# Performance work log

Hardware: AMD Instinct MI355X
Metric: run time of the kernel (lower is better)

## Reference

```python
import jax, jax.numpy as jnp
import numpy as np

E, D, H, B = 8, 64, 512, 32768  # n_experts, state_dim, hidden width, batch
IN = D + 3  # x, t, sin(omega*t), cos(omega*t)


def setup_inputs() -> dict:
    key = jax.random.key(0)
    ks = jax.random.split(key, 12)
    s = 0.02
    return {
        "t": jax.random.uniform(ks[0], (1,), dtype=jnp.float32),
        "x": jax.random.normal(ks[1], (B, D), dtype=jnp.float32),
        "expert_weights": jax.random.uniform(ks[2], (B, E), dtype=jnp.float32),
        "omega": jnp.arange(1, E + 1, dtype=jnp.float32),  # omega_i = i+1
        "W1": jax.random.normal(ks[3], (E, H, IN), dtype=jnp.float32) * s,
        "b1": jnp.zeros((E, H), dtype=jnp.float32),
        "W2": jax.random.normal(ks[4], (E, H, H), dtype=jnp.float32) * s,
        "b2": jnp.zeros((E, H), dtype=jnp.float32),
        "W3": jax.random.normal(ks[5], (E, H, H), dtype=jnp.float32) * s,
        "b3": jnp.zeros((E, H), dtype=jnp.float32),
        "W4": jax.random.normal(ks[6], (E, D, H), dtype=jnp.float32) * s,
        "b4": jnp.zeros((E, D), dtype=jnp.float32),
    }


def reference(t, x, expert_weights, omega, W1, b1, W2, b2, W3, b3, W4, b4):
    # Dense path of ExpertODEEnsemble.forward: all experts active.
    nB = x.shape[0]
    tb = jnp.broadcast_to(t, (nB,))                       # (B,)
    wt = omega[:, None] * tb[None, :]                     # (E, B)
    # Per-expert inputs: [x, t, sin(wt), cos(wt)] -> (E, B, D+3)
    xe = jnp.broadcast_to(x[None], (E, nB, D))
    te = jnp.broadcast_to(tb[None, :, None], (E, nB, 1))
    inp = jnp.concatenate([xe, te, jnp.sin(wt)[..., None], jnp.cos(wt)[..., None]], axis=-1)
    h = jnp.tanh(jnp.einsum('ebi,ehi->ebh', inp, W1) + b1[:, None, :])
    h = jnp.tanh(jnp.einsum('ebh,egh->ebg', h, W2) + b2[:, None, :])
    h = jnp.tanh(jnp.einsum('ebh,egh->ebg', h, W3) + b3[:, None, :])
    dyn = jnp.einsum('ebh,edh->ebd', h, W4) + b4[:, None, :]   # (E, B, D)
    # Weighted combine: sum_e w[b,e] * dyn[e,b,:]
    dx_dt = jnp.einsum('be,ebd->bd', expert_weights, dyn)
    return dx_dt
```

## Files before the change

### kernel.cpp

```cpp
#include <hip/hip_runtime.h>
#include <hip/hip_bf16.h>


typedef unsigned short ushort_t;
typedef unsigned int u32;
typedef unsigned long long u64;
typedef __attribute__((ext_vector_type(8))) short short8;
typedef __attribute__((ext_vector_type(4))) float floatx4;
typedef __attribute__((ext_vector_type(16))) float floatx16;
typedef __attribute__((ext_vector_type(4))) int intx4;

#define W1A_OFF 0u
#define W2A_OFF 524288u
#define W3A_OFF 4718592u
#define W4A_OFF 8912896u
#define XB_OFF  9437184u
#define B1E_OFF 13631488u

#define X_OFF_L 135168
#define SYNC_OFF 152064
#define SMEM_SZ 152128

static __device__ __forceinline__ u32 pk2bf(float a, float b) {
  union { __hip_bfloat162 h; u32 u; } v;
  v.h = __float22bfloat162_rn(make_float2(a, b));
  return v.u;
}

static __device__ __forceinline__ float pade_tanh(float x) {
  float x2 = x * x;
  float num = __builtin_fmaf(x2, __builtin_fmaf(x2, 1.0f, 105.0f), 945.0f);
  float den = __builtin_fmaf(x2, __builtin_fmaf(x2, 15.0f, 420.0f), 945.0f);
  return x * num * __builtin_amdgcn_rcpf(den);
}

static __device__ __forceinline__ void ald16(const void* g, void* l) {
  __builtin_amdgcn_global_load_lds((__attribute__((address_space(1))) void*)g,
                                   (__attribute__((address_space(3))) void*)l,
                                   16, 0, 0);
}

static __device__ __forceinline__ floatx16 mfma32(short8 a, short8 b, floatx16 c) {
  return __builtin_amdgcn_mfma_f32_32x32x16_bf16(a, b, c, 0, 0, 0);
}

static __device__ __forceinline__ void waitge(const int* p, int tgt) {
  while (*(volatile const int*)p < tgt) __builtin_amdgcn_s_sleep(1);
  __asm__ __volatile__("" ::: "memory");
}

static __device__ __forceinline__ void bump(int* p, int lane) {
  __asm__ __volatile__("s_waitcnt lgkmcnt(0)" ::: "memory");
  if (lane == 0) atomicAdd(p, 1);
}

__global__ __launch_bounds__(256) void prep_kernel(
    const float* __restrict__ t, const float* __restrict__ x,
    const float* __restrict__ omega, const float* __restrict__ W1,
    const float* __restrict__ b1, const float* __restrict__ W2,
    const float* __restrict__ W3, const float* __restrict__ W4,
    char* __restrict__ ws) {
  int i = blockIdx.x * 256 + threadIdx.x;
  if (i < 32768) {
    int e = i >> 12, d = i & 4095;
    int lane = d & 63, q = d >> 6;
    int ol = q & 1, kc = (q >> 1) & 3, w = q >> 3;
    int outr = w * 64 + ol * 32 + (lane & 31);
    int kg = kc * 2 + (lane >> 5);
    const float* s = W1 + (e * 512 + outr) * 67 + kg * 8;
    ((intx4*)(ws + W1A_OFF))[i] = (intx4){
        (int)pk2bf(s[0], s[1]), (int)pk2bf(s[2], s[3]),
        (int)pk2bf(s[4], s[5]), (int)pk2bf(s[6], s[7])};
    return;
  }
  i -= 32768;
  if (i < 262144) {
    int e = i >> 15, d = i & 32767;
    int lane = d & 63, q = d >> 6;
    int ol = q & 1, kc = (q >> 1) & 31, w = q >> 6;
    int outr = w * 64 + ol * 32 + (lane & 31);
    int kg = kc * 2 + (lane >> 5);
    const floatx4* s = (const floatx4*)(W2 + ((e << 9) + outr) * 512 + (kg << 3));
    floatx4 lo = s[0], hi = s[1];
    ((intx4*)(ws + W2A_OFF))[i] = (intx4){
        (int)pk2bf(lo[0], lo[1]), (int)pk2bf(lo[2], lo[3]),
        (int)pk2bf(hi[0], hi[1]), (int)pk2bf(hi[2], hi[3])};
    return;
  }
  i -= 262144;
  if (i < 262144) {
    int e = i >> 15, d = i & 32767;
    int lane = d & 63, q = d >> 6;
    int ol = q & 1, kc = (q >> 1) & 31, w = q >> 6;
    int outr = w * 64 + ol * 32 + (lane & 31);
    int kg = kc * 2 + (lane >> 5);
    const floatx4* s = (const floatx4*)(W3 + ((e << 9) + outr) * 512 + (kg << 3));
    floatx4 lo = s[0], hi = s[1];
    ((intx4*)(ws + W3A_OFF))[i] = (intx4){
        (int)pk2bf(lo[0], lo[1]), (int)pk2bf(lo[2], lo[3]),
        (int)pk2bf(hi[0], hi[1]), (int)pk2bf(hi[2], hi[3])};
    return;
  }
  i -= 262144;
  if (i < 32768) {
    int e = i >> 12, d = i & 4095;
    int lane = d & 63, q = d >> 6;
    int kc = q & 31, o4 = q >> 5;
    int outr = o4 * 32 + (lane & 31);
    int kg = kc * 2 + (lane >> 5);
    const floatx4* s = (const floatx4*)(W4 + ((e << 6) + outr) * 512 + (kg << 3));
    floatx4 lo = s[0], hi = s[1];
    ((intx4*)(ws + W4A_OFF))[i] = (intx4){
        (int)pk2bf(lo[0], lo[1]), (int)pk2bf(lo[2], lo[3]),
        (int)pk2bf(hi[0], hi[1]), (int)pk2bf(hi[2], hi[3])};
    return;
  }
  i -= 32768;
  if (i < 262144) {
    const floatx4* s = (const floatx4*)(x + i * 8);
    floatx4 lo = s[0], hi = s[1];
    ((intx4*)(ws + XB_OFF))[i] = (intx4){
        (int)pk2bf(lo[0], lo[1]), (int)pk2bf(lo[2], lo[3]),
        (int)pk2bf(hi[0], hi[1]), (int)pk2bf(hi[2], hi[3])};
    return;
  }
  i -= 262144;
  if (i < 4096) {
    float tv = t[0];
    int e = i >> 9;
    float om = omega[e];
    ((float*)(ws + B1E_OFF))[i] = b1[i] + tv * W1[i * 67 + 64]
        + sinf(om * tv) * W1[i * 67 + 65] + cosf(om * tv) * W1[i * 67 + 66];
  }
}


template <int NKC, bool ISX>
static __device__ __forceinline__ void mlp_layer(
    const char* __restrict__ bsrc, char* __restrict__ act,
    int* kcp, int* pub, int lane, int w, int q1, int r31,
    const char* __restrict__ Abase, const float* __restrict__ bias,
    int pub_tgt, int tgt_cov, int tgt_oth, int khm, bool do_epi_wait) {
  const int voff = lane * 16;
  const char* sp = Abase + w * (NKC * 2048) + voff;

  floatx16 acc[2][4];
#pragma unroll
  for (int ol = 0; ol < 2; ++ol) {
    int fe0 = w * 64 + ol * 32 + 4 * q1;
#pragma unroll
    for (int g = 0; g < 4; ++g) {
      floatx4 bv = *(const floatx4*)(bias + fe0 + 8 * g);
#pragma unroll
      for (int nt = 0; nt < 4; ++nt) {
        acc[ol][nt][4 * g + 0] = bv[0];
        acc[ol][nt][4 * g + 1] = bv[1];
        acc[ol][nt][4 * g + 2] = bv[2];
        acc[ol][nt][4 * g + 3] = bv[3];
      }
    }
  }
  short8 a0 = *(const short8*)(sp);
  short8 a1 = *(const short8*)(sp + 1024);
  sp += 2048;

  const int NG = NKC / 4;
#pragma unroll 1
  for (int g = 0; g < NG; ++g) {
    if (!ISX) waitge(pub + g, pub_tgt);
    const char* gb = bsrc + g * (4 * 4224) + voff;
    short8 b0 = *(const short8*)(gb);
    short8 b1v = *(const short8*)(gb + 1024);
    short8 b2 = *(const short8*)(gb + 2048);
    short8 b3 = *(const short8*)(gb + 3072);
#pragma unroll
    for (int j = 0; j < 4; ++j) {
      short8 an0 = *(const short8*)(sp);
      short8 an1 = *(const short8*)(sp + 1024);
      sp += 2048;
      const char* bn = gb + ((j + 1) & 3) * 4224;
      short8 bn0 = *(const short8*)(bn);
      short8 bn1 = *(const short8*)(bn + 1024);
      short8 bn2 = *(const short8*)(bn + 2048);
      short8 bn3 = *(const short8*)(bn + 3072);
      acc[0][0] = mfma32(a0, b0, acc[0][0]);
      acc[0][1] = mfma32(a0, b1v, acc[0][1]);
      acc[0][2] = mfma32(a0, b2, acc[0][2]);
      acc[0][3] = mfma32(a0, b3, acc[0][3]);
      acc[1][0] = mfma32(a1, b0, acc[1][0]);
      acc[1][1] = mfma32(a1, b1v, acc[1][1]);
      acc[1][2] = mfma32(a1, b2, acc[1][2]);
      acc[1][3] = mfma32(a1, b3, acc[1][3]);
      a0 = an0; a1 = an1;
      b0 = bn0; b1v = bn1; b2 = bn2; b3 = bn3;
    }
    bump(kcp + w, lane);
  }

  if (do_epi_wait) {
    for (int w2 = 0; w2 < 8; ++w2)
      waitge(kcp + w2, ((w2 >> 2) == khm) ? tgt_cov : tgt_oth);
  }
#pragma unroll
  for (int ol = 0; ol < 2; ++ol) {
#pragma unroll
    for (int g = 0; g < 4; ++g) {
      int ko = ol * 4 + g;
      char* base = act + (4 * w + (ko >> 1)) * 4224
                   + (((ko & 1) * 32 + r31) << 4) + q1 * 8;
#pragma unroll
      for (int nt = 0; nt < 4; ++nt) {
        float v0 = pade_tanh(acc[ol][nt][4 * g + 0]);
        float v1 = pade_tanh(acc[ol][nt][4 * g + 1]);
        float v2 = pade_tanh(acc[ol][nt][4 * g + 2]);
        float v3 = pade_tanh(acc[ol][nt][4 * g + 3]);
        u32 lo = pk2bf(v0, v1), hi = pk2bf(v2, v3);
        *(u64*)(base + nt * 1024) = ((u64)hi << 32) | lo;
      }
    }
  }
  bump(pub + w, lane);
}

extern "C" __global__ __launch_bounds__(512) void fused_kernel(
    const char* __restrict__ ws, const float* __restrict__ b2,
    const float* __restrict__ b3, const float* __restrict__ b4,
    const float* __restrict__ ew, float* __restrict__ out) {
  extern __shared__ char smem[];
  char* act = smem;
  char* xreg = smem + X_OFF_L;
  int* kcp = (int*)(smem + SYNC_OFF);
  int* pub = kcp + 8;

  const int t = threadIdx.x, lane = t & 63, w = t >> 6;
  const int q1 = lane >> 5, r31 = lane & 31;
  const int row0 = blockIdx.x << 7;
  const int voff = lane * 16;

  if (t < 16) ((int*)(smem + SYNC_OFF))[t] = 0;

  const ushort_t* xb = (const ushort_t*)(ws + XB_OFF);
#pragma unroll
  for (int s = 0; s < 2; ++s) {
    int u = w + 8 * s, v = u >> 2, nt = u & 3;
    ald16(xb + (row0 + nt * 32 + r31) * 64 + (2 * v + q1) * 8,
          xreg + v * 4224 + nt * 1024);
  }
  __syncthreads();

  const int rt = w & 3, kh = w >> 2;
  const int row_l4 = row0 + rt * 32 + r31;
  floatx16 oacc[2] = {};

  for (int e = 0; e < 8; ++e) {
    mlp_layer<4, true>(xreg, act, kcp, pub, lane, w, q1, r31,
                       ws + W1A_OFF + e * 65536,
                       (const float*)(ws + B1E_OFF) + e * 512,
                       0, 21 * e + (w & 3) - 3, 21 * e + w - 11, w >> 2, e > 0);
    mlp_layer<32, false>(act, act, kcp, pub, lane, w, q1, r31,
                         ws + W2A_OFF + e * 524288, b2 + e * 512,
                         3 * e + 1, 21 * e + w + 2, 21 * e + w + 2, 0, true);
    mlp_layer<32, false>(act, act, kcp, pub, lane, w, q1, r31,
                         ws + W3A_OFF + e * 524288, b3 + e * 512,
                         3 * e + 2, 21 * e + w + 10, 21 * e + w + 10, 0, true);

    {
      const char* spA = ws + W4A_OFF + e * 65536 + voff;
      const float sc = ew[row_l4 * 8 + e];
      floatx16 acc4[2] = {};
      int kc0 = kh * 16;
      short8 a0 = *(const short8*)(spA + kc0 * 1024);
      short8 a1 = *(const short8*)(spA + 32768 + kc0 * 1024);
#pragma unroll 1
      for (int gl = 0; gl < 4; ++gl) {
        int g = kh * 4 + gl;
        waitge(pub + g, 3 * e + 3);
        const char* gb = act + g * (4 * 4224) + rt * 1024 + voff;
        short8 b = *(const short8*)(gb);
#pragma unroll
        for (int j = 0; j < 4; ++j) {
          int kc = g * 4 + j;
          short8 an0 = *(const short8*)(spA + (kc + 1) * 1024);
          short8 an1 = *(const short8*)(spA + 32768 + (kc + 1) * 1024);
          short8 bn = *(const short8*)(gb + ((j + 1) & 3) * 4224);
          acc4[0] = mfma32(a0, b, acc4[0]);
          acc4[1] = mfma32(a1, b, acc4[1]);
          a0 = an0; a1 = an1; b = bn;
        }
        bump(kcp + w, lane);
      }
      if (kh == 0) {
        const float* bp = b4 + e * 64;
#pragma unroll
        for (int ol = 0; ol < 2; ++ol) {
          int fe0 = ol * 32 + 4 * q1;
#pragma unroll
          for (int g = 0; g < 4; ++g) {
            floatx4 bv = *(const floatx4*)(bp + fe0 + 8 * g);
            oacc[ol][4 * g + 0] += sc * (acc4[ol][4 * g + 0] + bv[0]);
            oacc[ol][4 * g + 1] += sc * (acc4[ol][4 * g + 1] + bv[1]);
            oacc[ol][4 * g + 2] += sc * (acc4[ol][4 * g + 2] + bv[2]);
            oacc[ol][4 * g + 3] += sc * (acc4[ol][4 * g + 3] + bv[3]);
          }
        }
      } else {
#pragma unroll
        for (int ol = 0; ol < 2; ++ol)
#pragma unroll
          for (int i = 0; i < 16; ++i) oacc[ol][i] += sc * acc4[ol][i];
      }
    }
  }

  __syncthreads();
  if (kh == 1) {
#pragma unroll
    for (int ol = 0; ol < 2; ++ol)
#pragma unroll
      for (int g = 0; g < 4; ++g) {
        floatx4 p = {oacc[ol][4 * g + 0], oacc[ol][4 * g + 1],
                     oacc[ol][4 * g + 2], oacc[ol][4 * g + 3]};
        *(floatx4*)(act + rt * 8192 + ol * 4096 + g * 1024 + lane * 16) = p;
      }
  }
  __syncthreads();
  if (kh == 0) {
    float* orow = out + row_l4 * 64;
#pragma unroll
    for (int ol = 0; ol < 2; ++ol)
#pragma unroll
      for (int g = 0; g < 4; ++g) {
        floatx4 p = *(const floatx4*)(act + rt * 8192 + ol * 4096 + g * 1024 + lane * 16);
        floatx4 v = {oacc[ol][4 * g + 0] + p[0], oacc[ol][4 * g + 1] + p[1],
                     oacc[ol][4 * g + 2] + p[2], oacc[ol][4 * g + 3] + p[3]};
        *(floatx4*)(orow + ol * 32 + 8 * g + 4 * q1) = v;
      }
  }
}

extern "C" void kernel_launch(void* const* d_in, const int* in_sizes, int n_in,
                              void* d_out, int out_size, void* d_ws, size_t ws_size,
                              hipStream_t stream) {
  const float* t  = (const float*)d_in[0];
  const float* x  = (const float*)d_in[1];
  const float* ew = (const float*)d_in[2];
  const float* om = (const float*)d_in[3];
  const float* W1 = (const float*)d_in[4];
  const float* b1 = (const float*)d_in[5];
  const float* W2 = (const float*)d_in[6];
  const float* b2 = (const float*)d_in[7];
  const float* W3 = (const float*)d_in[8];
  const float* b3 = (const float*)d_in[9];
  const float* W4 = (const float*)d_in[10];
  const float* b4 = (const float*)d_in[11];
  char* ws = (char*)d_ws;
  float* out = (float*)d_out;
  (void)in_sizes; (void)n_in; (void)ws_size; (void)out_size;

  static int smem_set = 0;
  if (!smem_set) {
    hipFuncSetAttribute((const void*)fused_kernel,
                        hipFuncAttributeMaxDynamicSharedMemorySize, SMEM_SZ);
    smem_set = 1;
  }
  prep_kernel<<<3344, 256, 0, stream>>>(t, x, om, W1, b1, W2, W3, W4, ws);
  fused_kernel<<<256, 512, SMEM_SZ, stream>>>(ws, b2, b3, b4, ew, out);
}
```

Measured before the change: 431.3 us.

## Split fused MLP into 64-row, 4-wave blocks with two blocks per CU

The fused expert-MLP kernel now uses blocks of 256 threads covering 64 rows instead of 512 threads covering 128 rows. Each wave computes 128 output features against two 32-row tiles, and LDS use is roughly halved so two blocks fit per CU. The inter-wave counters and epilogue waits are reworked to match: the W4 stage reads only slabs the wave wrote itself, and the final cross-wave reduction sums four partials. The aim is better latency hiding through more resident blocks and less cross-wave waiting. The cost is twice as many blocks, each streaming the full bf16 weight set from L2, so weight reuse per block drops.

```diff
diff --git a/kernel.cpp b/kernel.cpp
--- a/kernel.cpp
+++ b/kernel.cpp
@@ -17,9 +17,10 @@
 #define XB_OFF  9437184u
 #define B1E_OFF 13631488u
 
-#define X_OFF_L 135168
-#define SYNC_OFF 152064
-#define SMEM_SZ 152128
+#define SLAB 2112
+#define X_OFF_L 67584
+#define SYNC_OFF 76032
+#define SMEM_SZ 76096
 
 static __device__ __forceinline__ u32 pk2bf(float a, float b) {
   union { __hip_bfloat162 h; u32 u; } v;
@@ -134,25 +135,25 @@
   }
 }
 
-
-template <int NKC, bool ISX>
-static __device__ __forceinline__ void mlp_layer(
+template <int NKC, bool ISX, bool BUMP>
+static __device__ __forceinline__ void mlp_layer4(
     const char* __restrict__ bsrc, char* __restrict__ act,
     int* kcp, int* pub, int lane, int w, int q1, int r31,
     const char* __restrict__ Abase, const float* __restrict__ bias,
-    int pub_tgt, int tgt_cov, int tgt_oth, int khm, bool do_epi_wait) {
+    int pub_tgt, int epi_base, bool do_epi) {
   const int voff = lane * 16;
-  const char* sp = Abase + w * (NKC * 2048) + voff;
-
-  floatx16 acc[2][4];
-#pragma unroll
-  for (int ol = 0; ol < 2; ++ol) {
-    int fe0 = w * 64 + ol * 32 + 4 * q1;
+  const int AH = NKC * 2048;
+  const char* spA = Abase + (2 * w) * AH + voff;
+
+  floatx16 acc[4][2];
+#pragma unroll
+  for (int ol = 0; ol < 4; ++ol) {
+    int fe0 = w * 128 + ol * 32 + 4 * q1;
 #pragma unroll
     for (int g = 0; g < 4; ++g) {
       floatx4 bv = *(const floatx4*)(bias + fe0 + 8 * g);
 #pragma unroll
-      for (int nt = 0; nt < 4; ++nt) {
+      for (int nt = 0; nt < 2; ++nt) {
         acc[ol][nt][4 * g + 0] = bv[0];
         acc[ol][nt][4 * g + 1] = bv[1];
         acc[ol][nt][4 * g + 2] = bv[2];
@@ -160,56 +161,56 @@
       }
     }
   }
-  short8 a0 = *(const short8*)(sp);
-  short8 a1 = *(const short8*)(sp + 1024);
-  sp += 2048;
+  short8 a0 = *(const short8*)(spA);
+  short8 a1 = *(const short8*)(spA + 1024);
+  short8 a2 = *(const short8*)(spA + AH);
+  short8 a3 = *(const short8*)(spA + AH + 1024);
+  spA += 2048;
 
   const int NG = NKC / 4;
 #pragma unroll 1
   for (int g = 0; g < NG; ++g) {
-    if (!ISX) waitge(pub + g, pub_tgt);
-    const char* gb = bsrc + g * (4 * 4224) + voff;
+    if (!ISX) waitge(pub + (g >> 1), pub_tgt);
+    const char* gb = bsrc + g * (4 * SLAB) + voff;
     short8 b0 = *(const short8*)(gb);
     short8 b1v = *(const short8*)(gb + 1024);
-    short8 b2 = *(const short8*)(gb + 2048);
-    short8 b3 = *(const short8*)(gb + 3072);
 #pragma unroll
     for (int j = 0; j < 4; ++j) {
-      short8 an0 = *(const short8*)(sp);
-      short8 an1 = *(const short8*)(sp + 1024);
-      sp += 2048;
-      const char* bn = gb + ((j + 1) & 3) * 4224;
+      short8 an0 = *(const short8*)(spA);
+      short8 an1 = *(const short8*)(spA + 1024);
+      short8 an2 = *(const short8*)(spA + AH);
+      short8 an3 = *(const short8*)(spA + AH + 1024);
+      spA += 2048;
+      const char* bn = gb + ((j + 1) & 3) * SLAB;
       short8 bn0 = *(const short8*)(bn);
       short8 bn1 = *(const short8*)(bn + 1024);
-      short8 bn2 = *(const short8*)(bn + 2048);
-      short8 bn3 = *(const short8*)(bn + 3072);
       acc[0][0] = mfma32(a0, b0, acc[0][0]);
       acc[0][1] = mfma32(a0, b1v, acc[0][1]);
-      acc[0][2] = mfma32(a0, b2, acc[0][2]);
-      acc[0][3] = mfma32(a0, b3, acc[0][3]);
       acc[1][0] = mfma32(a1, b0, acc[1][0]);
       acc[1][1] = mfma32(a1, b1v, acc[1][1]);
-      acc[1][2] = mfma32(a1, b2, acc[1][2]);
-      acc[1][3] = mfma32(a1, b3, acc[1][3]);
-      a0 = an0; a1 = an1;
-      b0 = bn0; b1v = bn1; b2 = bn2; b3 = bn3;
-    }
-    bump(kcp + w, lane);
-  }
-
-  if (do_epi_wait) {
-    for (int w2 = 0; w2 < 8; ++w2)
-      waitge(kcp + w2, ((w2 >> 2) == khm) ? tgt_cov : tgt_oth);
-  }
-#pragma unroll
-  for (int ol = 0; ol < 2; ++ol) {
+      acc[2][0] = mfma32(a2, b0, acc[2][0]);
+      acc[2][1] = mfma32(a2, b1v, acc[2][1]);
+      acc[3][0] = mfma32(a3, b0, acc[3][0]);
+      acc[3][1] = mfma32(a3, b1v, acc[3][1]);
+      a0 = an0; a1 = an1; a2 = an2; a3 = an3;
+      b0 = bn0; b1v = bn1;
+    }
+    if (BUMP) bump(kcp + w, lane);
+  }
+
+  if (do_epi) {
+#pragma unroll 1
+    for (int w2 = 0; w2 < 4; ++w2) waitge(kcp + w2, epi_base + 2 * w + 2);
+  }
+#pragma unroll
+  for (int ol = 0; ol < 4; ++ol) {
 #pragma unroll
     for (int g = 0; g < 4; ++g) {
       int ko = ol * 4 + g;
-      char* base = act + (4 * w + (ko >> 1)) * 4224
+      char* base = act + (8 * w + (ko >> 1)) * SLAB
                    + (((ko & 1) * 32 + r31) << 4) + q1 * 8;
 #pragma unroll
-      for (int nt = 0; nt < 4; ++nt) {
+      for (int nt = 0; nt < 2; ++nt) {
         float v0 = pade_tanh(acc[ol][nt][4 * g + 0]);
         float v1 = pade_tanh(acc[ol][nt][4 * g + 1]);
         float v2 = pade_tanh(acc[ol][nt][4 * g + 2]);
@@ -222,7 +223,7 @@
   bump(pub + w, lane);
 }
 
-extern "C" __global__ __launch_bounds__(512) void fused_kernel(
+extern "C" __global__ __launch_bounds__(256, 2) void fused_kernel(
     const char* __restrict__ ws, const float* __restrict__ b2,
     const float* __restrict__ b3, const float* __restrict__ b4,
     const float* __restrict__ ew, float* __restrict__ out) {
@@ -230,111 +231,119 @@
   char* act = smem;
   char* xreg = smem + X_OFF_L;
   int* kcp = (int*)(smem + SYNC_OFF);
-  int* pub = kcp + 8;
+  int* pub = kcp + 4;
 
   const int t = threadIdx.x, lane = t & 63, w = t >> 6;
   const int q1 = lane >> 5, r31 = lane & 31;
-  const int row0 = blockIdx.x << 7;
+  const int row0 = blockIdx.x << 6;
   const int voff = lane * 16;
 
-  if (t < 16) ((int*)(smem + SYNC_OFF))[t] = 0;
+  if (t < 8) ((int*)(smem + SYNC_OFF))[t] = 0;
 
   const ushort_t* xb = (const ushort_t*)(ws + XB_OFF);
 #pragma unroll
   for (int s = 0; s < 2; ++s) {
-    int u = w + 8 * s, v = u >> 2, nt = u & 3;
+    int u = w + 4 * s, v = u >> 1, nt = u & 1;
     ald16(xb + (row0 + nt * 32 + r31) * 64 + (2 * v + q1) * 8,
-          xreg + v * 4224 + nt * 1024);
+          xreg + v * SLAB + nt * 1024);
   }
   __syncthreads();
 
-  const int rt = w & 3, kh = w >> 2;
-  const int row_l4 = row0 + rt * 32 + r31;
-  floatx16 oacc[2] = {};
+  floatx16 oacc[2][2] = {};
 
   for (int e = 0; e < 8; ++e) {
-    mlp_layer<4, true>(xreg, act, kcp, pub, lane, w, q1, r31,
-                       ws + W1A_OFF + e * 65536,
-                       (const float*)(ws + B1E_OFF) + e * 512,
-                       0, 21 * e + (w & 3) - 3, 21 * e + w - 11, w >> 2, e > 0);
-    mlp_layer<32, false>(act, act, kcp, pub, lane, w, q1, r31,
-                         ws + W2A_OFF + e * 524288, b2 + e * 512,
-                         3 * e + 1, 21 * e + w + 2, 21 * e + w + 2, 0, true);
-    mlp_layer<32, false>(act, act, kcp, pub, lane, w, q1, r31,
-                         ws + W3A_OFF + e * 524288, b3 + e * 512,
-                         3 * e + 2, 21 * e + w + 10, 21 * e + w + 10, 0, true);
+    mlp_layer4<4, true, false>(xreg, act, kcp, pub, lane, w, q1, r31,
+                               ws + W1A_OFF + e * 65536,
+                               (const float*)(ws + B1E_OFF) + e * 512,
+                               0, 0, false);
+    mlp_layer4<32, false, true>(act, act, kcp, pub, lane, w, q1, r31,
+                                ws + W2A_OFF + e * 524288, b2 + e * 512,
+                                3 * e + 1, 16 * e, true);
+    mlp_layer4<32, false, true>(act, act, kcp, pub, lane, w, q1, r31,
+                                ws + W3A_OFF + e * 524288, b3 + e * 512,
+                                3 * e + 2, 16 * e + 8, true);
 
     {
       const char* spA = ws + W4A_OFF + e * 65536 + voff;
-      const float sc = ew[row_l4 * 8 + e];
-      floatx16 acc4[2] = {};
-      int kc0 = kh * 16;
+      floatx16 acc4[2][2] = {};
+      const int kc0 = 8 * w;
       short8 a0 = *(const short8*)(spA + kc0 * 1024);
-      short8 a1 = *(const short8*)(spA + 32768 + kc0 * 1024);
+      short8 a1 = *(const short8*)(spA + (32 + kc0) * 1024);
 #pragma unroll 1
-      for (int gl = 0; gl < 4; ++gl) {
-        int g = kh * 4 + gl;
-        waitge(pub + g, 3 * e + 3);
-        const char* gb = act + g * (4 * 4224) + rt * 1024 + voff;
-        short8 b = *(const short8*)(gb);
+      for (int gl = 0; gl < 2; ++gl) {
+        int g = 2 * w + gl;
+        const char* gb = act + g * (4 * SLAB) + voff;
+        short8 b0 = *(const short8*)(gb);
+        short8 b1v = *(const short8*)(gb + 1024);
 #pragma unroll
         for (int j = 0; j < 4; ++j) {
-          int kc = g * 4 + j;
+          int kc = kc0 + gl * 4 + j;
           short8 an0 = *(const short8*)(spA + (kc + 1) * 1024);
-          short8 an1 = *(const short8*)(spA + 32768 + (kc + 1) * 1024);
-          short8 bn = *(const short8*)(gb + ((j + 1) & 3) * 4224);
-          acc4[0] = mfma32(a0, b, acc4[0]);
-          acc4[1] = mfma32(a1, b, acc4[1]);
-          a0 = an0; a1 = an1; b = bn;
+          short8 an1 = *(const short8*)(spA + (33 + kc) * 1024);
+          const char* bn = gb + ((j + 1) & 3) * SLAB;
+          short8 bn0 = *(const short8*)(bn);
+          short8 bn1 = *(const short8*)(bn + 1024);
+          acc4[0][0] = mfma32(a0, b0, acc4[0][0]);
+          acc4[0][1] = mfma32(a0, b1v, acc4[0][1]);
+          acc4[1][0] = mfma32(a1, b0, acc4[1][0]);
+          acc4[1][1] = mfma32(a1, b1v, acc4[1][1]);
+          a0 = an0; a1 = an1; b0 = bn0; b1v = bn1;
         }
-        bump(kcp + w, lane);
-      }
-      if (kh == 0) {
-        const float* bp = b4 + e * 64;
-#pragma unroll
-        for (int ol = 0; ol < 2; ++ol) {
-          int fe0 = ol * 32 + 4 * q1;
-#pragma unroll
-          for (int g = 0; g < 4; ++g) {
-            floatx4 bv = *(const floatx4*)(bp + fe0 + 8 * g);
-            oacc[ol][4 * g + 0] += sc * (acc4[ol][4 * g + 0] + bv[0]);
-            oacc[ol][4 * g + 1] += sc * (acc4[ol][4 * g + 1] + bv[1]);
-            oacc[ol][4 * g + 2] += sc * (acc4[ol][4 * g + 2] + bv[2]);
-            oacc[ol][4 * g + 3] += sc * (acc4[ol][4 * g + 3] + bv[3]);
+      }
+#pragma unroll
+      for (int nt = 0; nt < 2; ++nt) {
+        const float sc = ew[(row0 + nt * 32 + r31) * 8 + e];
+        if (w == 0) {
+          const float* bp = b4 + e * 64;
+#pragma unroll
+          for (int o4 = 0; o4 < 2; ++o4) {
+            int fe0 = o4 * 32 + 4 * q1;
+#pragma unroll
+            for (int g = 0; g < 4; ++g) {
+              floatx4 bv = *(const floatx4*)(bp + fe0 + 8 * g);
+              oacc[o4][nt][4 * g + 0] += sc * (acc4[o4][nt][4 * g + 0] + bv[0]);
+              oacc[o4][nt][4 * g + 1] += sc * (acc4[o4][nt][4 * g + 1] + bv[1]);
+              oacc[o4][nt][4 * g + 2] += sc * (acc4[o4][nt][4 * g + 2] + bv[2]);
+              oacc[o4][nt][4 * g + 3] += sc * (acc4[o4][nt][4 * g + 3] + bv[3]);
+            }
           }
+        } else {
+#pragma unroll
+          for (int o4 = 0; o4 < 2; ++o4)
+#pragma unroll
+            for (int i = 0; i < 16; ++i)
+              oacc[o4][nt][i] += sc * acc4[o4][nt][i];
         }
-      } else {
-#pragma unroll
-        for (int ol = 0; ol < 2; ++ol)
-#pragma unroll
-          for (int i = 0; i < 16; ++i) oacc[ol][i] += sc * acc4[ol][i];
       }
     }
   }
 
   __syncthreads();
-  if (kh == 1) {
-#pragma unroll
-    for (int ol = 0; ol < 2; ++ol)
+#pragma unroll
+  for (int o4 = 0; o4 < 2; ++o4)
+#pragma unroll
+    for (int nt = 0; nt < 2; ++nt)
 #pragma unroll
       for (int g = 0; g < 4; ++g) {
-        floatx4 p = {oacc[ol][4 * g + 0], oacc[ol][4 * g + 1],
-                     oacc[ol][4 * g + 2], oacc[ol][4 * g + 3]};
-        *(floatx4*)(act + rt * 8192 + ol * 4096 + g * 1024 + lane * 16) = p;
-      }
-  }
+        floatx4 p = {oacc[o4][nt][4 * g + 0], oacc[o4][nt][4 * g + 1],
+                     oacc[o4][nt][4 * g + 2], oacc[o4][nt][4 * g + 3]};
+        *(floatx4*)(act + (w * 4096 + (nt * 32 + r31) * 64
+                           + o4 * 32 + g * 8 + q1 * 4) * 4) = p;
+      }
   __syncthreads();
-  if (kh == 0) {
-    float* orow = out + row_l4 * 64;
-#pragma unroll
-    for (int ol = 0; ol < 2; ++ol)
-#pragma unroll
-      for (int g = 0; g < 4; ++g) {
-        floatx4 p = *(const floatx4*)(act + rt * 8192 + ol * 4096 + g * 1024 + lane * 16);
-        floatx4 v = {oacc[ol][4 * g + 0] + p[0], oacc[ol][4 * g + 1] + p[1],
-                     oacc[ol][4 * g + 2] + p[2], oacc[ol][4 * g + 3] + p[3]};
-        *(floatx4*)(orow + ol * 32 + 8 * g + 4 * q1) = v;
-      }
+  {
+    float* orow = out + row0 * 64;
+#pragma unroll
+    for (int k = 0; k < 4; ++k) {
+      int f = w * 1024 + k * 256 + lane * 4;
+      floatx4 s0 = *(const floatx4*)(act + f * 4);
+      floatx4 s1 = *(const floatx4*)(act + (4096 + f) * 4);
+      floatx4 s2 = *(const floatx4*)(act + (8192 + f) * 4);
+      floatx4 s3 = *(const floatx4*)(act + (12288 + f) * 4);
+      floatx4 v = {s0[0] + s1[0] + s2[0] + s3[0], s0[1] + s1[1] + s2[1] + s3[1],
+                   s0[2] + s1[2] + s2[2] + s3[2], s0[3] + s1[3] + s2[3] + s3[3]};
+      *(floatx4*)(orow + f) = v;
+    }
   }
 }
 
@@ -364,5 +373,5 @@
     smem_set = 1;
   }
   prep_kernel<<<3344, 256, 0, stream>>>(t, x, om, W1, b1, W2, W3, W4, ws);
-  fused_kernel<<<256, 512, SMEM_SZ, stream>>>(ws, b2, b3, b4, ew, out);
-}
+  fused_kernel<<<512, 256, SMEM_SZ, stream>>>(ws, b2, b3, b4, ew, out);
+}
```

New measurement: 686.7 us. +59.2%, slower.

## Rotate activation buffers across nine LDS slots with staggered per-wave K order

Applied to the files above, without the earlier changes.

Replaces the in-place activation buffer with a nine-slot rotating LDS ring, so each layer writes into a fresh slot and no longer waits for every wave to finish reading the previous one. Each wave starts its K loop at its own published group and walks backward, using finer per-group counters and vectorised guard checks in place of full barrier-like waits. Layer 1 now reads x directly from global memory instead of staging it in LDS. MFMA issue is raised with setprio and waves are staggered at start with sleeps. The synchronisation protocol is intricate and raises the risk of races or deadlock.

```diff
diff --git a/kernel.cpp b/kernel.cpp
--- a/kernel.cpp
+++ b/kernel.cpp
@@ -17,9 +17,9 @@
 #define XB_OFF  9437184u
 #define B1E_OFF 13631488u
 
-#define X_OFF_L 135168
-#define SYNC_OFF 152064
-#define SMEM_SZ 152128
+#define SLOTB 16384
+#define SYNC_OFF 147456
+#define SMEM_SZ 147552
 
 static __device__ __forceinline__ u32 pk2bf(float a, float b) {
   union { __hip_bfloat162 h; u32 u; } v;
@@ -34,14 +34,14 @@
   return x * num * __builtin_amdgcn_rcpf(den);
 }
 
-static __device__ __forceinline__ void ald16(const void* g, void* l) {
-  __builtin_amdgcn_global_load_lds((__attribute__((address_space(1))) void*)g,
-                                   (__attribute__((address_space(3))) void*)l,
-                                   16, 0, 0);
-}
-
 static __device__ __forceinline__ floatx16 mfma32(short8 a, short8 b, floatx16 c) {
   return __builtin_amdgcn_mfma_f32_32x32x16_bf16(a, b, c, 0, 0, 0);
+}
+
+static __device__ __forceinline__ int slot9(int g, int b) {
+  int s = g + b;
+  if (s >= 9) s -= 9;
+  return s * SLOTB;
 }
 
 static __device__ __forceinline__ void waitge(const int* p, int tgt) {
@@ -49,8 +49,43 @@
   __asm__ __volatile__("" ::: "memory");
 }
 
+static __device__ __forceinline__ void waitge4(const int* p, int tgt) {
+  for (;;) {
+    __asm__ __volatile__("" ::: "memory");
+    intx4 v = *(const intx4*)p;
+    if (v[0] >= tgt && v[1] >= tgt && v[2] >= tgt && v[3] >= tgt) break;
+    __builtin_amdgcn_s_sleep(1);
+  }
+  __asm__ __volatile__("" ::: "memory");
+}
+
+static __device__ __forceinline__ void guard_grp(const int* grp, int w, int base) {
+  int tg0 = base + ((0 - w - 1) & 7) + 1;
+  int tg1 = base + ((1 - w - 1) & 7) + 1;
+  int tg2 = base + ((2 - w - 1) & 7) + 1;
+  int tg3 = base + ((3 - w - 1) & 7) + 1;
+  int tg4 = base + ((4 - w - 1) & 7) + 1;
+  int tg5 = base + ((5 - w - 1) & 7) + 1;
+  int tg6 = base + ((6 - w - 1) & 7) + 1;
+  int tg7 = base + ((7 - w - 1) & 7) + 1;
+  for (;;) {
+    __asm__ __volatile__("" ::: "memory");
+    intx4 a = *(const intx4*)grp;
+    intx4 b = *(const intx4*)(grp + 4);
+    if (a[0] >= tg0 && a[1] >= tg1 && a[2] >= tg2 && a[3] >= tg3 &&
+        b[0] >= tg4 && b[1] >= tg5 && b[2] >= tg6 && b[3] >= tg7) break;
+    __builtin_amdgcn_s_sleep(1);
+  }
+  __asm__ __volatile__("" ::: "memory");
+}
+
 static __device__ __forceinline__ void bump(int* p, int lane) {
   __asm__ __volatile__("s_waitcnt lgkmcnt(0)" ::: "memory");
+  if (lane == 0) atomicAdd(p, 1);
+}
+
+static __device__ __forceinline__ void bump_sig(int* p, int lane) {
+  __builtin_amdgcn_sched_barrier(0);
   if (lane == 0) atomicAdd(p, 1);
 }
 
@@ -135,14 +170,35 @@
 }
 
 
-template <int NKC, bool ISX>
-static __device__ __forceinline__ void mlp_layer(
-    const char* __restrict__ bsrc, char* __restrict__ act,
-    int* kcp, int* pub, int lane, int w, int q1, int r31,
+static __device__ __forceinline__ void epi_write(
+    floatx16 acc[2][4], char* __restrict__ act, int wbyte, int r31, int q1) {
+#pragma unroll
+  for (int ol = 0; ol < 2; ++ol) {
+#pragma unroll
+    for (int g = 0; g < 4; ++g) {
+      int ko = ol * 4 + g;
+      char* base = act + wbyte + (ko >> 1) * 4096
+                   + (((ko & 1) * 32 + r31) << 4) + q1 * 8;
+#pragma unroll
+      for (int nt = 0; nt < 4; ++nt) {
+        float v0 = pade_tanh(acc[ol][nt][4 * g + 0]);
+        float v1 = pade_tanh(acc[ol][nt][4 * g + 1]);
+        float v2 = pade_tanh(acc[ol][nt][4 * g + 2]);
+        float v3 = pade_tanh(acc[ol][nt][4 * g + 3]);
+        u32 lo = pk2bf(v0, v1), hi = pk2bf(v2, v3);
+        *(u64*)(base + nt * 1024) = ((u64)hi << 32) | lo;
+      }
+    }
+  }
+}
+
+static __device__ __forceinline__ void mlp_l1(
+    char* __restrict__ act, int* pub, int* l4c, int* grp,
+    int lane, int w, int q1, int r31,
     const char* __restrict__ Abase, const float* __restrict__ bias,
-    int pub_tgt, int tgt_cov, int tgt_oth, int khm, bool do_epi_wait) {
+    const char* __restrict__ xl, int wbyte, int e) {
   const int voff = lane * 16;
-  const char* sp = Abase + w * (NKC * 2048) + voff;
+  const char* ap = Abase + w * 8192 + voff;
 
   floatx16 acc[2][4];
 #pragma unroll
@@ -160,29 +216,105 @@
       }
     }
   }
-  short8 a0 = *(const short8*)(sp);
-  short8 a1 = *(const short8*)(sp + 1024);
-  sp += 2048;
-
-  const int NG = NKC / 4;
+  short8 b0 = *(const short8*)(xl);
+  short8 b1v = *(const short8*)(xl + 4096);
+  short8 b2 = *(const short8*)(xl + 8192);
+  short8 b3 = *(const short8*)(xl + 12288);
+  short8 a0 = *(const short8*)(ap);
+  short8 a1 = *(const short8*)(ap + 1024);
+
+#pragma unroll
+  for (int j = 0; j < 4; ++j) {
+    int kcn = (j < 3) ? (j + 1) : 3;
+    const char* xn = xl + kcn * 32;
+    const char* apn = (j < 3) ? (ap + 2048) : ap;
+    short8 an0 = *(const short8*)(apn);
+    short8 an1 = *(const short8*)(apn + 1024);
+    short8 bn0 = *(const short8*)(xn);
+    short8 bn1 = *(const short8*)(xn + 4096);
+    short8 bn2 = *(const short8*)(xn + 8192);
+    short8 bn3 = *(const short8*)(xn + 12288);
+    __builtin_amdgcn_s_setprio(1);
+    acc[0][0] = mfma32(a0, b0, acc[0][0]);
+    acc[0][1] = mfma32(a0, b1v, acc[0][1]);
+    acc[0][2] = mfma32(a0, b2, acc[0][2]);
+    acc[0][3] = mfma32(a0, b3, acc[0][3]);
+    acc[1][0] = mfma32(a1, b0, acc[1][0]);
+    acc[1][1] = mfma32(a1, b1v, acc[1][1]);
+    acc[1][2] = mfma32(a1, b2, acc[1][2]);
+    acc[1][3] = mfma32(a1, b3, acc[1][3]);
+    __builtin_amdgcn_s_setprio(0);
+    a0 = an0; a1 = an1;
+    b0 = bn0; b1v = bn1; b2 = bn2; b3 = bn3;
+    ap = apn;
+  }
+  if (e > 0) {
+    if (w < 7) waitge4(l4c + ((w + 1) >> 2) * 4, e);
+    else       guard_grp(grp, w, 16 * e - 8);
+  }
+  epi_write(acc, act, wbyte, r31, q1);
+  bump(pub + w, lane);
+}
+
+static __device__ __forceinline__ void mlp_mid(
+    char* __restrict__ act, int* pub, int* grp, int lane, int w, int q1, int r31,
+    const char* __restrict__ Abase, const float* __restrict__ bias,
+    int pub_tgt, int rbase9, int wbyte, int gmode, int garg,
+    const int* __restrict__ l4p) {
+  const int voff = lane * 16;
+  const char* spA = Abase + w * 65536 + voff;
+
+  floatx16 acc[2][4];
+#pragma unroll
+  for (int ol = 0; ol < 2; ++ol) {
+    int fe0 = w * 64 + ol * 32 + 4 * q1;
+#pragma unroll
+    for (int g = 0; g < 4; ++g) {
+      floatx4 bv = *(const floatx4*)(bias + fe0 + 8 * g);
+#pragma unroll
+      for (int nt = 0; nt < 4; ++nt) {
+        acc[ol][nt][4 * g + 0] = bv[0];
+        acc[ol][nt][4 * g + 1] = bv[1];
+        acc[ol][nt][4 * g + 2] = bv[2];
+        acc[ol][nt][4 * g + 3] = bv[3];
+      }
+    }
+  }
+  const char* gb = act + slot9(w, rbase9) + voff;
+  const char* ap = spA + (4 * w) * 2048;
+  short8 b0 = *(const short8*)(gb);
+  short8 b1v = *(const short8*)(gb + 1024);
+  short8 b2 = *(const short8*)(gb + 2048);
+  short8 b3 = *(const short8*)(gb + 3072);
+  short8 a0 = *(const short8*)(ap);
+  short8 a1 = *(const short8*)(ap + 1024);
+
 #pragma unroll 1
-  for (int g = 0; g < NG; ++g) {
-    if (!ISX) waitge(pub + g, pub_tgt);
-    const char* gb = bsrc + g * (4 * 4224) + voff;
-    short8 b0 = *(const short8*)(gb);
-    short8 b1v = *(const short8*)(gb + 1024);
-    short8 b2 = *(const short8*)(gb + 2048);
-    short8 b3 = *(const short8*)(gb + 3072);
+  for (int i = 0; i < 8; ++i) {
 #pragma unroll
     for (int j = 0; j < 4; ++j) {
-      short8 an0 = *(const short8*)(sp);
-      short8 an1 = *(const short8*)(sp + 1024);
-      sp += 2048;
-      const char* bn = gb + ((j + 1) & 3) * 4224;
-      short8 bn0 = *(const short8*)(bn);
-      short8 bn1 = *(const short8*)(bn + 1024);
-      short8 bn2 = *(const short8*)(bn + 2048);
-      short8 bn3 = *(const short8*)(bn + 3072);
+      const char* apn;
+      const char* gbn = gb;
+      const char* bsl;
+      if (j < 3) {
+        apn = ap + 2048;
+        bsl = gb + (j + 1) * 4096;
+      } else if (i < 7) {
+        int g2 = (w - i - 1) & 7;
+        waitge(pub + g2, pub_tgt);
+        gbn = act + slot9(g2, rbase9) + voff;
+        apn = spA + (4 * g2) * 2048;
+        bsl = gbn;
+      } else {
+        apn = ap; bsl = gb;
+      }
+      short8 an0 = *(const short8*)(apn);
+      short8 an1 = *(const short8*)(apn + 1024);
+      short8 bn0 = *(const short8*)(bsl);
+      short8 bn1 = *(const short8*)(bsl + 1024);
+      short8 bn2 = *(const short8*)(bsl + 2048);
+      short8 bn3 = *(const short8*)(bsl + 3072);
+      __builtin_amdgcn_s_setprio(1);
       acc[0][0] = mfma32(a0, b0, acc[0][0]);
       acc[0][1] = mfma32(a0, b1v, acc[0][1]);
       acc[0][2] = mfma32(a0, b2, acc[0][2]);
@@ -191,34 +323,17 @@
       acc[1][1] = mfma32(a1, b1v, acc[1][1]);
       acc[1][2] = mfma32(a1, b2, acc[1][2]);
       acc[1][3] = mfma32(a1, b3, acc[1][3]);
+      __builtin_amdgcn_s_setprio(0);
       a0 = an0; a1 = an1;
       b0 = bn0; b1v = bn1; b2 = bn2; b3 = bn3;
+      ap = apn; gb = gbn;
     }
-    bump(kcp + w, lane);
-  }
-
-  if (do_epi_wait) {
-    for (int w2 = 0; w2 < 8; ++w2)
-      waitge(kcp + w2, ((w2 >> 2) == khm) ? tgt_cov : tgt_oth);
-  }
-#pragma unroll
-  for (int ol = 0; ol < 2; ++ol) {
-#pragma unroll
-    for (int g = 0; g < 4; ++g) {
-      int ko = ol * 4 + g;
-      char* base = act + (4 * w + (ko >> 1)) * 4224
-                   + (((ko & 1) * 32 + r31) << 4) + q1 * 8;
-#pragma unroll
-      for (int nt = 0; nt < 4; ++nt) {
-        float v0 = pade_tanh(acc[ol][nt][4 * g + 0]);
-        float v1 = pade_tanh(acc[ol][nt][4 * g + 1]);
-        float v2 = pade_tanh(acc[ol][nt][4 * g + 2]);
-        float v3 = pade_tanh(acc[ol][nt][4 * g + 3]);
-        u32 lo = pk2bf(v0, v1), hi = pk2bf(v2, v3);
-        *(u64*)(base + nt * 1024) = ((u64)hi << 32) | lo;
-      }
-    }
-  }
+    bump_sig(grp + w, lane);
+  }
+
+  if (gmode == 1)      guard_grp(grp, w, garg);
+  else if (gmode == 2) waitge4(l4p, garg);
+  epi_write(acc, act, wbyte, r31, q1);
   bump(pub + w, lane);
 }
 
@@ -228,79 +343,99 @@
     const float* __restrict__ ew, float* __restrict__ out) {
   extern __shared__ char smem[];
   char* act = smem;
-  char* xreg = smem + X_OFF_L;
-  int* kcp = (int*)(smem + SYNC_OFF);
-  int* pub = kcp + 8;
+  int* l4c = (int*)(smem + SYNC_OFF);
+  int* pub = l4c + 8;
+  int* grp = l4c + 16;
 
   const int t = threadIdx.x, lane = t & 63, w = t >> 6;
   const int q1 = lane >> 5, r31 = lane & 31;
   const int row0 = blockIdx.x << 7;
   const int voff = lane * 16;
 
-  if (t < 16) ((int*)(smem + SYNC_OFF))[t] = 0;
-
-  const ushort_t* xb = (const ushort_t*)(ws + XB_OFF);
-#pragma unroll
-  for (int s = 0; s < 2; ++s) {
-    int u = w + 8 * s, v = u >> 2, nt = u & 3;
-    ald16(xb + (row0 + nt * 32 + r31) * 64 + (2 * v + q1) * 8,
-          xreg + v * 4224 + nt * 1024);
-  }
+  if (t < 24) ((int*)(smem + SYNC_OFF))[t] = 0;
   __syncthreads();
+
+  for (int i = (7 - w) * 7; i > 0; --i) __builtin_amdgcn_s_sleep(1);
+
+  const char* xl = (const char*)ws + XB_OFF + (size_t)row0 * 128
+                   + r31 * 128 + q1 * 16;
 
   const int rt = w & 3, kh = w >> 2;
   const int row_l4 = row0 + rt * 32 + r31;
   floatx16 oacc[2] = {};
 
   for (int e = 0; e < 8; ++e) {
-    mlp_layer<4, true>(xreg, act, kcp, pub, lane, w, q1, r31,
-                       ws + W1A_OFF + e * 65536,
-                       (const float*)(ws + B1E_OFF) + e * 512,
-                       0, 21 * e + (w & 3) - 3, 21 * e + w - 11, w >> 2, e > 0);
-    mlp_layer<32, false>(act, act, kcp, pub, lane, w, q1, r31,
-                         ws + W2A_OFF + e * 524288, b2 + e * 512,
-                         3 * e + 1, 21 * e + w + 2, 21 * e + w + 2, 0, true);
-    mlp_layer<32, false>(act, act, kcp, pub, lane, w, q1, r31,
-                         ws + W3A_OFF + e * 524288, b3 + e * 512,
-                         3 * e + 2, 21 * e + w + 10, 21 * e + w + 10, 0, true);
+    int l0 = 3 * e;
+    int s1 = (l0 + 1) % 9, s2 = (l0 + 2) % 9, s3 = (l0 + 3) % 9;
+
+    mlp_l1(act, pub, l4c, grp, lane, w, q1, r31,
+           (const char*)ws + W1A_OFF + e * 65536,
+           (const float*)(ws + B1E_OFF) + e * 512, xl, slot9(w, s1), e);
+    mlp_mid(act, pub, grp, lane, w, q1, r31,
+            (const char*)ws + W2A_OFF + e * 524288, b2 + e * 512,
+            3 * e + 1, s1, slot9(w, s2),
+            (w < 7) ? 1 : ((e > 0) ? 2 : 0),
+            (w < 7) ? 16 * e : e, l4c);
+    mlp_mid(act, pub, grp, lane, w, q1, r31,
+            (const char*)ws + W3A_OFF + e * 524288, b3 + e * 512,
+            3 * e + 2, s2, slot9(w, s3),
+            1, (w < 7) ? 16 * e + 8 : 16 * e, l4c);
 
     {
-      const char* spA = ws + W4A_OFF + e * 65536 + voff;
+      const char* spA4 = (const char*)ws + W4A_OFF + e * 65536 + voff;
       const float sc = ew[row_l4 * 8 + e];
       floatx16 acc4[2] = {};
-      int kc0 = kh * 16;
-      short8 a0 = *(const short8*)(spA + kc0 * 1024);
-      short8 a1 = *(const short8*)(spA + 32768 + kc0 * 1024);
+      int g = 4 * kh + 3;
+      waitge(pub + g, 3 * e + 3);
+      const char* agb = spA4 + (4 * g) * 1024;
+      const char* gb = act + slot9(g, s3) + rt * 1024 + voff;
+      short8 a0 = *(const short8*)(agb);
+      short8 a1 = *(const short8*)(agb + 32768);
+      short8 b = *(const short8*)(gb);
 #pragma unroll 1
       for (int gl = 0; gl < 4; ++gl) {
-        int g = kh * 4 + gl;
-        waitge(pub + g, 3 * e + 3);
-        const char* gb = act + g * (4 * 4224) + rt * 1024 + voff;
-        short8 b = *(const short8*)(gb);
 #pragma unroll
         for (int j = 0; j < 4; ++j) {
-          int kc = g * 4 + j;
-          short8 an0 = *(const short8*)(spA + (kc + 1) * 1024);
-          short8 an1 = *(const short8*)(spA + 32768 + (kc + 1) * 1024);
-          short8 bn = *(const short8*)(gb + ((j + 1) & 3) * 4224);
+          const char* agn = agb;
+          const char* gbn = gb;
+          const char* asl; const char* bsl;
+          if (j < 3) {
+            asl = agb + (j + 1) * 1024;
+            bsl = gb + (j + 1) * 4096;
+          } else if (gl < 3) {
+            int g2 = g - 1;
+            waitge(pub + g2, 3 * e + 3);
+            agn = spA4 + (4 * g2) * 1024;
+            gbn = act + slot9(g2, s3) + rt * 1024 + voff;
+            asl = agn; bsl = gbn;
+          } else {
+            asl = agb; bsl = gb;
+          }
+          short8 an0 = *(const short8*)(asl);
+          short8 an1 = *(const short8*)(asl + 32768);
+          short8 bn = *(const short8*)(bsl);
+          __builtin_amdgcn_s_setprio(1);
           acc4[0] = mfma32(a0, b, acc4[0]);
           acc4[1] = mfma32(a1, b, acc4[1]);
+          __builtin_amdgcn_s_setprio(0);
           a0 = an0; a1 = an1; b = bn;
+          agb = agn; gb = gbn;
         }
-        bump(kcp + w, lane);
-      }
+        g = g - 1;
+      }
+      bump_sig(l4c + w, lane);
       if (kh == 0) {
         const float* bp = b4 + e * 64;
 #pragma unroll
         for (int ol = 0; ol < 2; ++ol) {
           int fe0 = ol * 32 + 4 * q1;
 #pragma unroll
-          for (int g = 0; g < 4; ++g) {
-            floatx4 bv = *(const floatx4*)(bp + fe0 + 8 * g);
-            oacc[ol][4 * g + 0] += sc * (acc4[ol][4 * g + 0] + bv[0]);
-            oacc[ol][4 * g + 1] += sc * (acc4[ol][4 * g + 1] + bv[1]);
-            oacc[ol][4 * g + 2] += sc * (acc4[ol][4 * g + 2] + bv[2]);
-            oacc[ol][4 * g + 3] += sc * (acc4[ol][4 * g + 3] + bv[3]);
+          for (int g2 = 0; g2 < 4; ++g2) {
+            floatx4 bv = *(const floatx4*)(bp + fe0 + 8 * g2);
+            oacc[ol][4 * g2 + 0] += sc * (acc4[ol][4 * g2 + 0] + bv[0]);
+            oacc[ol][4 * g2 + 1] += sc * (acc4[ol][4 * g2 + 1] + bv[1]);
+            oacc[ol][4 * g2 + 2] += sc * (acc4[ol][4 * g2 + 2] + bv[2]);
+            oacc[ol][4 * g2 + 3] += sc * (acc4[ol][4 * g2 + 3] + bv[3]);
           }
         }
       } else {
@@ -325,7 +460,7 @@
   }
   __syncthreads();
   if (kh == 0) {
-    float* orow = out + row_l4 * 64;
+    float* orow = out + (size_t)row_l4 * 64;
 #pragma unroll
     for (int ol = 0; ol < 2; ++ol)
 #pragma unroll
```

Result: slower. 461.3 us (+7.0%).
